# Optimization experiments

Measured on AMD Instinct MI355X. Metric: run time of the kernel, lower is better.

Reference implementation:

```python
import jax, jax.numpy as jnp
import numpy as np

N_NODES = 4096
N_EDGES = 65536
BS = 16
LEAKY_SLOPE = 0.01
BN_EPS = 1e-5


def _init(key, shape, scale=0.02):
    return (jax.random.normal(key, shape, dtype=jnp.float32) * scale)


def setup_inputs() -> dict:
    key = jax.random.key(0)
    ks = jax.random.split(key, 20)
    x_in = jax.random.normal(ks[0], (N_NODES, 8500), dtype=jnp.float32)
    edge_index = jax.random.randint(ks[1], (2, N_EDGES), 0, N_NODES, dtype=jnp.int64)
    return {
        "x_in": x_in,
        "edge_index": edge_index,
        # SAGEConv params: Wl (neighbor lin, with bias), Wr (root lin, no bias)
        "W1l": _init(ks[2], (320, 8500)), "b1": jnp.zeros((320,), jnp.float32), "W1r": _init(ks[3], (320, 8500)),
        "W2l": _init(ks[4], (180, 320)),  "b2": jnp.zeros((180,), jnp.float32), "W2r": _init(ks[5], (180, 320)),
        "W3l": _init(ks[6], (90, 180)),   "b3": jnp.zeros((90,), jnp.float32),  "W3r": _init(ks[7], (90, 180)),
        "W4l": _init(ks[8], (50, 90)),    "b4": jnp.zeros((50,), jnp.float32),  "W4r": _init(ks[9], (50, 90)),
        "Wf1": _init(ks[10], (32, 50)),   "bf1": jnp.zeros((32,), jnp.float32),
        "Wf2": _init(ks[11], (16, 32)),   "bf2": jnp.zeros((16,), jnp.float32),
        "Wf3": _init(ks[12], (1, 16)),    "bf3": jnp.zeros((1,), jnp.float32),
    }


def _sage(x, src, dst, Wl, bl, Wr):
    # PyG SAGEConv: out = lin_l(mean_{j in N(i)} x_j) + lin_r(x_i)
    agg = jax.ops.segment_sum(x[src], dst, num_segments=N_NODES)          # [N, F]
    deg = jax.ops.segment_sum(jnp.ones_like(dst, dtype=x.dtype), dst, num_segments=N_NODES)
    mean = agg / jnp.maximum(deg, 1.0)[:, None]
    return mean @ Wl.T + bl + x @ Wr.T


def _leaky(x):
    return jnp.where(x >= 0, x, LEAKY_SLOPE * x)


def _bn(x):
    # F.batch_norm(x, None, None, training=True): per-feature, biased var, no affine
    m = jnp.mean(x, axis=0)
    v = jnp.mean((x - m) ** 2, axis=0)
    return (x - m) / jnp.sqrt(v + BN_EPS)


def reference(x_in, edge_index,
              W1l, b1, W1r, W2l, b2, W2r, W3l, b3, W3r, W4l, b4, W4r,
              Wf1, bf1, Wf2, bf2, Wf3, bf3):
    src, dst = edge_index[0], edge_index[1]
    x = _bn(_leaky(_sage(x_in, src, dst, W1l, b1, W1r)))
    x = _bn(_leaky(_sage(x, src, dst, W2l, b2, W2r)))
    x = _bn(_leaky(_sage(x, src, dst, W3l, b3, W3r)))
    x = _bn(_leaky(_sage(x, src, dst, W4l, b4, W4r)))
    # get_batch: label i -> floor(i / (N/BS)); global_add_pool == segment sum
    x = x.reshape(BS, N_NODES // BS, -1).sum(axis=1)                      # [BS, 50]
    x = x @ Wf1.T + bf1
    x = x @ Wf2.T + bf2
    x = x @ Wf3.T + bf3
    return x
```

## Files before the change

### kernel.cpp

```cpp
#include <hip/hip_runtime.h>
#include <stdint.h>

#define NN 4096
#define NE 65536
#define LEAKY 0.01f
#define BN_EPS 1e-5f
#define DSTRIDE 96

typedef float f32x4 __attribute__((ext_vector_type(4)));
typedef __bf16 bf16x8 __attribute__((ext_vector_type(8)));
typedef unsigned short u16x8 __attribute__((ext_vector_type(8)));
typedef unsigned short u16x4 __attribute__((ext_vector_type(4)));

static __device__ __forceinline__ unsigned short f2bf(float v) {
  unsigned int u = __float_as_uint(v);
  u += 0x7fff + ((u >> 16) & 1);
  return (unsigned short)(u >> 16);
}

static __device__ __forceinline__ f32x4 bf4f(u16x4 v) {
  f32x4 r;
#pragma unroll
  for (int j = 0; j < 4; ++j) r[j] = __uint_as_float(((unsigned)v[j]) << 16);
  return r;
}

typedef __attribute__((address_space(1))) void gvoid;
typedef __attribute__((address_space(3))) void lvoid;

static __device__ __forceinline__ void async16(const void* g, void* l) {
  __builtin_amdgcn_global_load_lds((gvoid*)(uintptr_t)g,
                                   (lvoid*)(uint32_t)(uintptr_t)l, 16, 0, 0);
}


static __device__ __forceinline__ void pack_w_seg(int lblk, const float* __restrict__ Wl,
                                                  const float* __restrict__ Wr,
                                                  unsigned short* __restrict__ dst,
                                                  int Fout, int Fin, int Kp, int Np) {
  int nb = Kp >> 3;
  int idx = lblk * 256 + threadIdx.x;
  if (idx >= Np * nb) return;
  int row = idx / nb, kb = idx - row * nb;
  int g = kb >> 3, b = kb & 7;
  int dkb = (g << 3) | ((b + row) & 7);
  const float* src = nullptr;
  if (row < Fout)          src = Wl + (size_t)row * Fin;
  else if (row < 2 * Fout) src = Wr + (size_t)(row - Fout) * Fin;
  u16x8 st;
#pragma unroll
  for (int o = 0; o < 8; ++o) {
    int k = kb * 8 + o;
    float v = (src && k < Fin) ? src[k] : 0.f;
    st[o] = f2bf(v);
  }
  *(u16x8*)&dst[(size_t)row * Kp + dkb * 8] = st;
}

#define ADJ_BLK    256
#define PW1_BLK   2660
#define PW2_BLK     60
#define PW3_BLK     24
#define PW4_BLK      8
#define SETUP_BLK (ADJ_BLK + PW1_BLK + PW2_BLK + PW3_BLK + PW4_BLK)

__global__ __launch_bounds__(256) void setup_all(
    const int* __restrict__ esrc, const int* __restrict__ edst,
    const float* __restrict__ W1l, const float* __restrict__ W1r,
    const float* __restrict__ W2l, const float* __restrict__ W2r,
    const float* __restrict__ W3l, const float* __restrict__ W3r,
    const float* __restrict__ W4l, const float* __restrict__ W4r,
    unsigned short* __restrict__ wb1, unsigned short* __restrict__ wb2,
    unsigned short* __restrict__ wb3, unsigned short* __restrict__ wb4,
    int* __restrict__ deg, int* __restrict__ eix) {
  int blk = blockIdx.x;
  if (blk < ADJ_BLK) {
    int e = blk * 256 + threadIdx.x;
    int d = edst[e];
    int pos = atomicAdd(&deg[d], 1);
    if (pos < DSTRIDE) eix[(size_t)d * DSTRIDE + pos] = esrc[e];
  } else if (blk < ADJ_BLK + PW1_BLK) {
    pack_w_seg(blk - ADJ_BLK, W1l, W1r, wb1, 320, 8500, 8512, 640);
  } else if (blk < ADJ_BLK + PW1_BLK + PW2_BLK) {
    pack_w_seg(blk - ADJ_BLK - PW1_BLK, W2l, W2r, wb2, 180, 320, 320, 384);
  } else if (blk < ADJ_BLK + PW1_BLK + PW2_BLK + PW3_BLK) {
    pack_w_seg(blk - ADJ_BLK - PW1_BLK - PW2_BLK, W3l, W3r, wb3, 90, 180, 192, 256);
  } else {
    pack_w_seg(blk - ADJ_BLK - PW1_BLK - PW2_BLK - PW3_BLK, W4l, W4r, wb4,
               50, 90, 128, 128);
  }
}

__global__ __launch_bounds__(256) void gemm_f32a(const float* __restrict__ X,
                                                 const unsigned short* __restrict__ B,
                                                 float* __restrict__ C, int N, int M) {
  const int K = 8512, KS = 133, FIN = 8500;
  __shared__ unsigned short smem[3 * 128 * 64];
  unsigned short* As = smem;

  const int t = threadIdx.x;
  const int bm = blockIdx.x, bn = blockIdx.y;
  const int lane = t & 63;
  const int wave = t >> 6;
  const int wm = (wave & 1) * 64, wn = (wave >> 1) * 64;
  const int l16 = lane & 15, quad = lane >> 4;

  const int gz = (int)gridDim.z, z = (int)blockIdx.z;
  const int per = KS / gz, rem = KS % gz;
  const int k0 = z * per + (z < rem ? z : rem);
  const int k1 = k0 + per + (z < rem ? 1 : 0);

  f32x4 acc[4][4];
#pragma unroll
  for (int i = 0; i < 4; ++i)
#pragma unroll
    for (int j = 0; j < 4; ++j) acc[i][j] = (f32x4){0.f, 0.f, 0.f, 0.f};

  const int srow = t >> 3;
  const int bblk = t & 7;
  const int scol = bblk * 8;
  const float* Xb = X + (size_t)(bm * 128) * FIN;
  const unsigned short* Bbase = B + (size_t)(bn * 128) * K + scol;

  float va[4][8];
  auto loadA = [&](int kt) {
    int gc = kt * 64 + scol;
#pragma unroll
    for (int p = 0; p < 4; ++p) {
      const float* ap = Xb + (size_t)(p * 32 + srow) * FIN + gc;
      if (gc + 8 <= FIN) {
        f32x4 a = *(const f32x4*)ap;
        f32x4 b2 = *(const f32x4*)(ap + 4);
#pragma unroll
        for (int o = 0; o < 4; ++o) { va[p][o] = a[o]; va[p][o + 4] = b2[o]; }
      } else {
#pragma unroll
        for (int o = 0; o < 8; ++o) va[p][o] = (gc + o < FIN) ? ap[o] : 0.f;
      }
    }
  };
  auto writeA = [&]() {
#pragma unroll
    for (int p = 0; p < 4; ++p) {
      int row = p * 32 + srow;
      int rot = ((bblk + row) & 7) * 8;
      bf16x8 bv;
#pragma unroll
      for (int o = 0; o < 8; ++o) bv[o] = (__bf16)va[p][o];
      *(bf16x8*)&As[row * 64 + rot] = bv;
    }
  };
  auto stageB = [&](int kt, int bb) {
    unsigned short* Bd = smem + 128 * 64 + bb * 128 * 64;
#pragma unroll
    for (int p = 0; p < 4; ++p) {
      int row = p * 32 + srow;
      async16(Bbase + (size_t)row * K + kt * 64, &Bd[row * 64 + scol]);
    }
  };

  loadA(k0);
  stageB(k0, 0);
  writeA();
  __syncthreads();

  int bb = 0;
  for (int kt = k0; kt < k1; ++kt) {
    bool more = (kt + 1 < k1);
    if (more) {
      loadA(kt + 1);
      stageB(kt + 1, bb ^ 1);
    }
    const unsigned short* Bs = smem + 128 * 64 + bb * 128 * 64;
#pragma unroll
    for (int kh = 0; kh < 2; ++kh) {
      const int s8 = ((kh * 4 + quad + l16) & 7) * 8;
      bf16x8 af[4], bfr[4];
#pragma unroll
      for (int i = 0; i < 4; ++i)
        af[i] = *(const bf16x8*)&As[(wm + i * 16 + l16) * 64 + s8];
#pragma unroll
      for (int j = 0; j < 4; ++j)
        bfr[j] = *(const bf16x8*)&Bs[(wn + j * 16 + l16) * 64 + s8];
#pragma unroll
      for (int i = 0; i < 4; ++i)
#pragma unroll
        for (int j = 0; j < 4; ++j)
          acc[i][j] = __builtin_amdgcn_mfma_f32_16x16x32_bf16(af[i], bfr[j], acc[i][j], 0, 0, 0);
    }
    __syncthreads();
    if (more) {
      writeA();
      __syncthreads();
      bb ^= 1;
    }
  }

  float* Cb = C + (size_t)blockIdx.z * M * N;
#pragma unroll
  for (int i = 0; i < 4; ++i) {
    int rbase = bm * 128 + wm + i * 16 + quad * 4;
#pragma unroll
    for (int j = 0; j < 4; ++j) {
      int col = bn * 128 + wn + j * 16 + l16;
      float* cp = Cb + (size_t)rbase * N + col;
#pragma unroll
      for (int r = 0; r < 4; ++r) cp[(size_t)r * N] = acc[i][j][r];
    }
  }
}

__global__ __launch_bounds__(256) void gemm_bt(const unsigned short* __restrict__ A,
                                               const unsigned short* __restrict__ B,
                                               unsigned short* __restrict__ C, int N,
                                               int K, int M) {
  __shared__ unsigned short smem[2 * 128 * 64];
  unsigned short* As = smem;
  unsigned short* Bs = smem + 128 * 64;

  const int t = threadIdx.x;
  const int bm = blockIdx.x, bn = blockIdx.y;
  const int lane = t & 63;
  const int wave = t >> 6;
  const int wm = (wave & 1) * 64, wn = (wave >> 1) * 64;
  const int l16 = lane & 15, quad = lane >> 4;

  const int ksteps = K >> 6;

  f32x4 acc[4][4];
#pragma unroll
  for (int i = 0; i < 4; ++i)
#pragma unroll
    for (int j = 0; j < 4; ++j) acc[i][j] = (f32x4){0.f, 0.f, 0.f, 0.f};

  const int srow = t >> 3;
  const int scol = (t & 7) * 8;
  const unsigned short* Abase = A + (size_t)(bm * 128) * K + scol;
  const unsigned short* Bbase = B + (size_t)(bn * 128) * K + scol;

  for (int kt = 0; kt < ksteps; ++kt) {
    const unsigned short* Ag = Abase + kt * 64;
    const unsigned short* Bg = Bbase + kt * 64;
#pragma unroll
    for (int p = 0; p < 4; ++p) {
      int row = p * 32 + srow;
      async16(Ag + (size_t)row * K, &As[row * 64 + scol]);
    }
#pragma unroll
    for (int p = 0; p < 4; ++p) {
      int row = p * 32 + srow;
      async16(Bg + (size_t)row * K, &Bs[row * 64 + scol]);
    }
    __syncthreads();
#pragma unroll
    for (int kh = 0; kh < 2; ++kh) {
      const int s8 = ((kh * 4 + quad + l16) & 7) * 8;
      bf16x8 af[4], bfr[4];
#pragma unroll
      for (int i = 0; i < 4; ++i)
        af[i] = *(const bf16x8*)&As[(wm + i * 16 + l16) * 64 + s8];
#pragma unroll
      for (int j = 0; j < 4; ++j)
        bfr[j] = *(const bf16x8*)&Bs[(wn + j * 16 + l16) * 64 + s8];
#pragma unroll
      for (int i = 0; i < 4; ++i)
#pragma unroll
        for (int j = 0; j < 4; ++j)
          acc[i][j] = __builtin_amdgcn_mfma_f32_16x16x32_bf16(af[i], bfr[j], acc[i][j], 0, 0, 0);
    }
    __syncthreads();
  }

#pragma unroll
  for (int i = 0; i < 4; ++i) {
    int rbase = bm * 128 + wm + i * 16 + quad * 4;
#pragma unroll
    for (int j = 0; j < 4; ++j) {
      int col = bn * 128 + wn + j * 16 + l16;
      unsigned short* cp = C + (size_t)rbase * N + col;
#pragma unroll
      for (int r = 0; r < 4; ++r) cp[(size_t)r * N] = f2bf(acc[i][j][r]);
    }
  }
}

__global__ void reduceNbf(const float* __restrict__ yp, unsigned short* __restrict__ y,
                          int nz) {
  int idx = blockIdx.x * 256 + threadIdx.x;
  const f32x4* p = (const f32x4*)yp;
  const int S = NN * 640 / 4;
  int i2 = idx * 2;
  f32x4 a = p[i2], b = p[i2 + 1];
  for (int sl = 1; sl < nz; ++sl) {
    a += p[i2 + (size_t)sl * S];
    b += p[i2 + 1 + (size_t)sl * S];
  }
  u16x8 st;
#pragma unroll
  for (int o = 0; o < 4; ++o) { st[o] = f2bf(a[o]); st[o + 4] = f2bf(b[o]); }
  *(u16x8*)&y[(size_t)idx * 8] = st;
}

__global__ __launch_bounds__(256) void sage_agg(
    const unsigned short* __restrict__ y, const int* __restrict__ deg,
    const int* __restrict__ eix, const float* __restrict__ bias,
    float* __restrict__ z, int F, int ldy) {
  int i = blockIdx.x;
  int tx = threadIdx.x, ty = threadIdx.y;
  __shared__ int se[DSTRIDE];
  __shared__ float red[3][64][4];
  int d = deg[i]; if (d > DSTRIDE) d = DSTRIDE;
  {
    int lt = ty * 64 + tx;
    if (lt < d) se[lt] = eix[(size_t)i * DSTRIDE + lt];
  }
  __syncthreads();
  int nfb = (F + 255) >> 8;
  for (int fb = 0; fb < nfb; ++fb) {
    int f4 = (fb * 64 + tx) * 4;
    bool active = (f4 < F);
    f32x4 s = {0.f, 0.f, 0.f, 0.f};
    if (active) {
      const unsigned short* yb = y + f4;
      int e = ty;
      for (; e + 4 < d; e += 8) {
        u16x4 a = *(const u16x4*)&yb[(size_t)se[e] * ldy];
        u16x4 b = *(const u16x4*)&yb[(size_t)se[e + 4] * ldy];
        s += bf4f(a); s += bf4f(b);
      }
      if (e < d) s += bf4f(*(const u16x4*)&yb[(size_t)se[e] * ldy]);
    }
    if (ty > 0) *(f32x4*)red[ty - 1][tx] = s;
    __syncthreads();
    if (ty == 0 && active) {
      s += *(const f32x4*)red[0][tx];
      s += *(const f32x4*)red[1][tx];
      s += *(const f32x4*)red[2][tx];
      float inv = 1.f / (float)(d > 1 ? d : 1);
      int cnt = F - f4; if (cnt > 4) cnt = 4;
      const unsigned short* yr = &y[(size_t)i * ldy + F + f4];
      float* zo = &z[(size_t)i * F + f4];
      for (int j = 0; j < cnt; ++j) {
        float rv = __uint_as_float(((unsigned)yr[j]) << 16);
        float w = s[j] * inv + rv + bias[f4 + j];
        zo[j] = (w >= 0.f) ? w : LEAKY * w;
      }
    }
    if (fb + 1 < nfb) __syncthreads();
  }
}


__global__ __launch_bounds__(256) void bn_part(const float* __restrict__ z,
                                               float* __restrict__ sums, int F) {
  int tx = threadIdx.x, ty = threadIdx.y;
  int f = blockIdx.x * 64 + tx;
  float s = 0.f, s2 = 0.f;
  if (f < F) {
    int r0 = blockIdx.y * 512 + ty * 128;
    for (int j = 0; j < 128; ++j) {
      float v = z[(size_t)(r0 + j) * F + f];
      s += v; s2 += v * v;
    }
  }
  __shared__ float ls[4][64], ls2[4][64];
  ls[ty][tx] = s; ls2[ty][tx] = s2;
  __syncthreads();
  if (ty == 0 && f < F) {
    float S  = ls[0][tx] + ls[1][tx] + ls[2][tx] + ls[3][tx];
    float S2 = ls2[0][tx] + ls2[1][tx] + ls2[2][tx] + ls2[3][tx];
    atomicAdd(&sums[f], S);
    atomicAdd(&sums[F + f], S2);
  }
}

__global__ void bn_norm8(const float* __restrict__ z, const float* __restrict__ sums,
                         unsigned short* __restrict__ xout, int F, int Kp) {
  int nb = Kp >> 3;
  int idx = blockIdx.x * 256 + threadIdx.x;
  int row = idx / nb, kb = idx - row * nb;
  int g = kb >> 3, b = kb & 7;
  int dkb = (g << 3) | ((b + row) & 7);
  u16x8 st;
#pragma unroll
  for (int o = 0; o < 8; ++o) {
    int k = kb * 8 + o;
    float v = 0.f;
    if (k < F) {
      float m  = sums[k] * (1.f / NN);
      float var = sums[F + k] * (1.f / NN) - m * m;
      float rs = rsqrtf(var + BN_EPS);
      v = (z[(size_t)row * F + k] - m) * rs;
    }
    st[o] = f2bf(v);
  }
  *(u16x8*)&xout[(size_t)row * Kp + dkb * 8] = st;
}

__global__ void pool_fc(const float* __restrict__ z,
                        const float* __restrict__ sums,
                        const float* __restrict__ Wf1, const float* __restrict__ bf1,
                        const float* __restrict__ Wf2, const float* __restrict__ bf2,
                        const float* __restrict__ Wf3, const float* __restrict__ bf3,
                        float* __restrict__ out) {
  __shared__ float ps[4][50];
  __shared__ float pool[50];
  __shared__ float h1[32], h2[16];
  int b = blockIdx.x, tx = threadIdx.x, ty = threadIdx.y;
  if (tx < 50) {
    float s = 0.f;
    int r0 = b * 256 + ty * 64;
    for (int r = 0; r < 64; ++r) s += z[(size_t)(r0 + r) * 50 + tx];
    ps[ty][tx] = s;
  }
  __syncthreads();
  if (ty == 0 && tx < 50) {
    float s = ps[0][tx] + ps[1][tx] + ps[2][tx] + ps[3][tx];
    float m  = sums[tx] * (1.f / NN);
    float var = sums[50 + tx] * (1.f / NN) - m * m;
    float rs = rsqrtf(var + BN_EPS);
    pool[tx] = (s - 256.f * m) * rs;
  }
  __syncthreads();
  if (ty == 0 && tx < 32) {
    float s = bf1[tx];
    for (int f = 0; f < 50; ++f) s += pool[f] * Wf1[tx * 50 + f];
    h1[tx] = s;
  }
  __syncthreads();
  if (ty == 0 && tx < 16) {
    float s = bf2[tx];
    for (int f = 0; f < 32; ++f) s += h1[f] * Wf2[tx * 32 + f];
    h2[tx] = s;
  }
  __syncthreads();
  if (ty == 0 && tx == 0) {
    float s = bf3[0];
    for (int f = 0; f < 16; ++f) s += h2[f] * Wf3[f];
    out[b] = s;
  }
}


extern "C" void kernel_launch(void* const* d_in, const int* in_sizes, int n_in,
                              void* d_out, int out_size, void* d_ws, size_t ws_size,
                              hipStream_t stream) {
  const float* x_in = (const float*)d_in[0];
  const int* ei = (const int*)d_in[1];
  const float* W1l = (const float*)d_in[2];
  const float* b1  = (const float*)d_in[3];
  const float* W1r = (const float*)d_in[4];
  const float* W2l = (const float*)d_in[5];
  const float* b2  = (const float*)d_in[6];
  const float* W2r = (const float*)d_in[7];
  const float* W3l = (const float*)d_in[8];
  const float* b3  = (const float*)d_in[9];
  const float* W3r = (const float*)d_in[10];
  const float* W4l = (const float*)d_in[11];
  const float* b4  = (const float*)d_in[12];
  const float* W4r = (const float*)d_in[13];
  const float* Wf1 = (const float*)d_in[14];
  const float* bf1 = (const float*)d_in[15];
  const float* Wf2 = (const float*)d_in[16];
  const float* bf2 = (const float*)d_in[17];
  const float* Wf3 = (const float*)d_in[18];
  const float* bf3 = (const float*)d_in[19];
  float* out = (float*)d_out;
  (void)in_sizes; (void)n_in; (void)out_size;

  char* ws = (char*)d_ws;
  size_t off = 0;
  auto alloc = [&](size_t bytes) -> void* {
    void* p = ws + off;
    off = (off + bytes + 255) & ~(size_t)255;
    return p;
  };
  unsigned short* xbf = (unsigned short*)alloc((size_t)NN * 320 * 2);
  unsigned short* wb1 = (unsigned short*)alloc((size_t)640 * 8512 * 2);
  unsigned short* wb2 = (unsigned short*)alloc((size_t)384 * 320 * 2);
  unsigned short* wb3 = (unsigned short*)alloc((size_t)256 * 192 * 2);
  unsigned short* wb4 = (unsigned short*)alloc((size_t)128 * 128 * 2);
  float* z    = (float*)alloc((size_t)NN * 320 * 4);
  int* deg    = (int*)alloc(NN * 4);
  float* bnsum = (float*)alloc(1280 * 4);
  int* eix    = (int*)alloc((size_t)NN * DSTRIDE * 4);
  unsigned short* ybf = (unsigned short*)alloc((size_t)NN * 640 * 2);
  const size_t YS = (size_t)NN * 640 * 4;
  float* yp = (float*)(ws + off);
  const int nz = 4;
  if (off + (size_t)nz * YS > ws_size) return;
  float* bns1 = bnsum;
  float* bns2 = bnsum + 640;
  float* bns3 = bnsum + 1000;
  float* bns4 = bnsum + 1180;

  hipMemsetAsync(deg, 0, NN * 4 + 1280 * 4, stream);

  setup_all<<<dim3(SETUP_BLK), dim3(256), 0, stream>>>(
      ei, ei + NE, W1l, W1r, W2l, W2r, W3l, W3r, W4l, W4r,
      wb1, wb2, wb3, wb4, deg, eix);

  gemm_f32a<<<dim3(32, 5, nz), dim3(256), 0, stream>>>(x_in, wb1, yp, 640, NN);
  reduceNbf<<<dim3(NN * 640 / 8 / 256), dim3(256), 0, stream>>>(yp, ybf, nz);
  sage_agg<<<dim3(NN), dim3(64, 4), 0, stream>>>(ybf, deg, eix, b1, z, 320, 640);
  bn_part<<<dim3(5, 8), dim3(64, 4), 0, stream>>>(z, bns1, 320);
  bn_norm8<<<dim3(NN * 40 / 256), dim3(256), 0, stream>>>(z, bns1, xbf, 320, 320);

  gemm_bt<<<dim3(32, 3, 1), dim3(256), 0, stream>>>(xbf, wb2, ybf, 384, 320, NN);
  sage_agg<<<dim3(NN), dim3(64, 4), 0, stream>>>(ybf, deg, eix, b2, z, 180, 384);
  bn_part<<<dim3(3, 8), dim3(64, 4), 0, stream>>>(z, bns2, 180);
  bn_norm8<<<dim3(NN * 24 / 256), dim3(256), 0, stream>>>(z, bns2, xbf, 180, 192);

  gemm_bt<<<dim3(32, 2, 1), dim3(256), 0, stream>>>(xbf, wb3, ybf, 256, 192, NN);
  sage_agg<<<dim3(NN), dim3(64, 4), 0, stream>>>(ybf, deg, eix, b3, z, 90, 256);
  bn_part<<<dim3(2, 8), dim3(64, 4), 0, stream>>>(z, bns3, 90);
  bn_norm8<<<dim3(NN * 16 / 256), dim3(256), 0, stream>>>(z, bns3, xbf, 90, 128);

  gemm_bt<<<dim3(32, 1, 1), dim3(256), 0, stream>>>(xbf, wb4, ybf, 128, 128, NN);
  sage_agg<<<dim3(NN), dim3(64, 4), 0, stream>>>(ybf, deg, eix, b4, z, 50, 128);
  bn_part<<<dim3(1, 8), dim3(64, 4), 0, stream>>>(z, bns4, 50);

  pool_fc<<<dim3(16), dim3(64, 4), 0, stream>>>(z, bns4, Wf1, bf1, Wf2, bf2, Wf3, bf3, out);
}
```

Before: 470.6 us.

## Fuse batch-norm statistics into SAGE aggregation via replicated atomics; widen split-K

The separate bn_part reduction kernels are removed. sage_agg now accumulates per-feature sum and sum-of-squares with global float atomics into 8 replicated buffers, chosen by node index, to spread contention. bn_norm8 and pool_fc combine the replicas, and bn_norm8 caches mean and inverse std in shared memory instead of recomputing them per element. The first-layer GEMM split-K factor also rises from 4 to 8 when the workspace allows. The aim is fewer launches and one less pass over z, at the cost of millions of contended atomics and a larger partial-sum reduction.

```diff
diff --git a/kernel.cpp b/kernel.cpp
--- a/kernel.cpp
+++ b/kernel.cpp
@@ -6,6 +6,8 @@
 #define LEAKY 0.01f
 #define BN_EPS 1e-5f
 #define DSTRIDE 96
+#define NREP 8
+#define REPSTRIDE 1280
 
 typedef float f32x4 __attribute__((ext_vector_type(4)));
 typedef __bf16 bf16x8 __attribute__((ext_vector_type(8)));
@@ -304,7 +306,7 @@
 __global__ __launch_bounds__(256) void sage_agg(
     const unsigned short* __restrict__ y, const int* __restrict__ deg,
     const int* __restrict__ eix, const float* __restrict__ bias,
-    float* __restrict__ z, int F, int ldy) {
+    float* __restrict__ z, float* __restrict__ sums, int F, int ldy) {
   int i = blockIdx.x;
   int tx = threadIdx.x, ty = threadIdx.y;
   __shared__ int se[DSTRIDE];
@@ -315,6 +317,7 @@
     if (lt < d) se[lt] = eix[(size_t)i * DSTRIDE + lt];
   }
   __syncthreads();
+  float* sr = sums + (size_t)(i & (NREP - 1)) * REPSTRIDE;
   int nfb = (F + 255) >> 8;
   for (int fb = 0; fb < nfb; ++fb) {
     int f4 = (fb * 64 + tx) * 4;
@@ -343,39 +346,32 @@
       for (int j = 0; j < cnt; ++j) {
         float rv = __uint_as_float(((unsigned)yr[j]) << 16);
         float w = s[j] * inv + rv + bias[f4 + j];
-        zo[j] = (w >= 0.f) ? w : LEAKY * w;
+        w = (w >= 0.f) ? w : LEAKY * w;
+        zo[j] = w;
+        atomicAdd(&sr[f4 + j], w);
+        atomicAdd(&sr[F + f4 + j], w * w);
       }
     }
     if (fb + 1 < nfb) __syncthreads();
-  }
-}
-
-
-__global__ __launch_bounds__(256) void bn_part(const float* __restrict__ z,
-                                               float* __restrict__ sums, int F) {
-  int tx = threadIdx.x, ty = threadIdx.y;
-  int f = blockIdx.x * 64 + tx;
-  float s = 0.f, s2 = 0.f;
-  if (f < F) {
-    int r0 = blockIdx.y * 512 + ty * 128;
-    for (int j = 0; j < 128; ++j) {
-      float v = z[(size_t)(r0 + j) * F + f];
-      s += v; s2 += v * v;
-    }
-  }
-  __shared__ float ls[4][64], ls2[4][64];
-  ls[ty][tx] = s; ls2[ty][tx] = s2;
-  __syncthreads();
-  if (ty == 0 && f < F) {
-    float S  = ls[0][tx] + ls[1][tx] + ls[2][tx] + ls[3][tx];
-    float S2 = ls2[0][tx] + ls2[1][tx] + ls2[2][tx] + ls2[3][tx];
-    atomicAdd(&sums[f], S);
-    atomicAdd(&sums[F + f], S2);
   }
 }
 
 __global__ void bn_norm8(const float* __restrict__ z, const float* __restrict__ sums,
                          unsigned short* __restrict__ xout, int F, int Kp) {
+  __shared__ float ms[320], rss[320];
+  for (int k = threadIdx.x; k < F; k += 256) {
+    float sm = 0.f, sq = 0.f;
+#pragma unroll
+    for (int r = 0; r < NREP; ++r) {
+      sm += sums[(size_t)r * REPSTRIDE + k];
+      sq += sums[(size_t)r * REPSTRIDE + F + k];
+    }
+    float m = sm * (1.f / NN);
+    float var = sq * (1.f / NN) - m * m;
+    ms[k] = m;
+    rss[k] = rsqrtf(var + BN_EPS);
+  }
+  __syncthreads();
   int nb = Kp >> 3;
   int idx = blockIdx.x * 256 + threadIdx.x;
   int row = idx / nb, kb = idx - row * nb;
@@ -386,12 +382,7 @@
   for (int o = 0; o < 8; ++o) {
     int k = kb * 8 + o;
     float v = 0.f;
-    if (k < F) {
-      float m  = sums[k] * (1.f / NN);
-      float var = sums[F + k] * (1.f / NN) - m * m;
-      float rs = rsqrtf(var + BN_EPS);
-      v = (z[(size_t)row * F + k] - m) * rs;
-    }
+    if (k < F) v = (z[(size_t)row * F + k] - ms[k]) * rss[k];
     st[o] = f2bf(v);
   }
   *(u16x8*)&xout[(size_t)row * Kp + dkb * 8] = st;
@@ -416,8 +407,14 @@
   __syncthreads();
   if (ty == 0 && tx < 50) {
     float s = ps[0][tx] + ps[1][tx] + ps[2][tx] + ps[3][tx];
-    float m  = sums[tx] * (1.f / NN);
-    float var = sums[50 + tx] * (1.f / NN) - m * m;
+    float sm = 0.f, sq = 0.f;
+#pragma unroll
+    for (int r = 0; r < NREP; ++r) {
+      sm += sums[(size_t)r * REPSTRIDE + tx];
+      sq += sums[(size_t)r * REPSTRIDE + 50 + tx];
+    }
+    float m  = sm * (1.f / NN);
+    float var = sq * (1.f / NN) - m * m;
     float rs = rsqrtf(var + BN_EPS);
     pool[tx] = (s - 256.f * m) * rs;
   }
@@ -482,19 +479,19 @@
   unsigned short* wb4 = (unsigned short*)alloc((size_t)128 * 128 * 2);
   float* z    = (float*)alloc((size_t)NN * 320 * 4);
   int* deg    = (int*)alloc(NN * 4);
-  float* bnsum = (float*)alloc(1280 * 4);
+  float* bnsum = (float*)alloc((size_t)NREP * REPSTRIDE * 4);
   int* eix    = (int*)alloc((size_t)NN * DSTRIDE * 4);
   unsigned short* ybf = (unsigned short*)alloc((size_t)NN * 640 * 2);
   const size_t YS = (size_t)NN * 640 * 4;
   float* yp = (float*)(ws + off);
-  const int nz = 4;
+  int nz = (off + 8 * YS <= ws_size) ? 8 : 4;
   if (off + (size_t)nz * YS > ws_size) return;
   float* bns1 = bnsum;
   float* bns2 = bnsum + 640;
   float* bns3 = bnsum + 1000;
   float* bns4 = bnsum + 1180;
 
-  hipMemsetAsync(deg, 0, NN * 4 + 1280 * 4, stream);
+  hipMemsetAsync(deg, 0, NN * 4 + (size_t)NREP * REPSTRIDE * 4, stream);
 
   setup_all<<<dim3(SETUP_BLK), dim3(256), 0, stream>>>(
       ei, ei + NE, W1l, W1r, W2l, W2r, W3l, W3r, W4l, W4r,
@@ -502,23 +499,19 @@
 
   gemm_f32a<<<dim3(32, 5, nz), dim3(256), 0, stream>>>(x_in, wb1, yp, 640, NN);
   reduceNbf<<<dim3(NN * 640 / 8 / 256), dim3(256), 0, stream>>>(yp, ybf, nz);
-  sage_agg<<<dim3(NN), dim3(64, 4), 0, stream>>>(ybf, deg, eix, b1, z, 320, 640);
-  bn_part<<<dim3(5, 8), dim3(64, 4), 0, stream>>>(z, bns1, 320);
+  sage_agg<<<dim3(NN), dim3(64, 4), 0, stream>>>(ybf, deg, eix, b1, z, bns1, 320, 640);
   bn_norm8<<<dim3(NN * 40 / 256), dim3(256), 0, stream>>>(z, bns1, xbf, 320, 320);
 
   gemm_bt<<<dim3(32, 3, 1), dim3(256), 0, stream>>>(xbf, wb2, ybf, 384, 320, NN);
-  sage_agg<<<dim3(NN), dim3(64, 4), 0, stream>>>(ybf, deg, eix, b2, z, 180, 384);
-  bn_part<<<dim3(3, 8), dim3(64, 4), 0, stream>>>(z, bns2, 180);
+  sage_agg<<<dim3(NN), dim3(64, 4), 0, stream>>>(ybf, deg, eix, b2, z, bns2, 180, 384);
   bn_norm8<<<dim3(NN * 24 / 256), dim3(256), 0, stream>>>(z, bns2, xbf, 180, 192);
 
   gemm_bt<<<dim3(32, 2, 1), dim3(256), 0, stream>>>(xbf, wb3, ybf, 256, 192, NN);
-  sage_agg<<<dim3(NN), dim3(64, 4), 0, stream>>>(ybf, deg, eix, b3, z, 90, 256);
-  bn_part<<<dim3(2, 8), dim3(64, 4), 0, stream>>>(z, bns3, 90);
+  sage_agg<<<dim3(NN), dim3(64, 4), 0, stream>>>(ybf, deg, eix, b3, z, bns3, 90, 256);
   bn_norm8<<<dim3(NN * 16 / 256), dim3(256), 0, stream>>>(z, bns3, xbf, 90, 128);
 
   gemm_bt<<<dim3(32, 1, 1), dim3(256), 0, stream>>>(xbf, wb4, ybf, 128, 128, NN);
-  sage_agg<<<dim3(NN), dim3(64, 4), 0, stream>>>(ybf, deg, eix, b4, z, 50, 128);
-  bn_part<<<dim3(1, 8), dim3(64, 4), 0, stream>>>(z, bns4, 50);
+  sage_agg<<<dim3(NN), dim3(64, 4), 0, stream>>>(ybf, deg, eix, b4, z, bns4, 50, 128);
 
   pool_fc<<<dim3(16), dim3(64, 4), 0, stream>>>(z, bns4, Wf1, bf1, Wf2, bf2, Wf3, bf3, out);
 }
```

Result: slower. 718.3 us (+52.6%).
